# Kernel optimization log

Measured on AMD Instinct MI355X. Metric: run time of the kernel, lower is better.

The kernel has to match this reference:

```python
import jax, jax.numpy as jnp
import numpy as np

B, N, F_IN, F_OUT = 4, 4096, 64, 64
ALPHA = 0.2   # leakyrelu negative slope
M_MIX = 0.8   # self.m
NEG_INF = -1e12


def setup_inputs() -> dict:
    key = jax.random.key(0)
    k1, k2, k3, k4 = jax.random.split(key, 4)
    inp = jax.random.normal(k1, (B, N, F_IN), dtype=jnp.float32)
    adj = jax.random.uniform(k2, (B, N, N), dtype=jnp.float32)
    # xavier_uniform with gain=1.414
    limW = 1.414 * np.sqrt(6.0 / (F_IN + F_OUT))
    W = jax.random.uniform(k3, (F_IN, F_OUT), dtype=jnp.float32, minval=-limW, maxval=limW)
    lima = 1.414 * np.sqrt(6.0 / (2 * F_OUT + 1))
    a = jax.random.uniform(k4, (2 * F_OUT, 1), dtype=jnp.float32, minval=-lima, maxval=lima)
    return {"inp": inp, "adj": adj, "W": W, "a": a}


def reference(inp, adj, W, a):
    # h: [B, N, F_OUT]
    h = jnp.einsum("bnf,fo->bno", inp, W)
    # The torch code builds a_input[b,i,j] = [h_i ; h_j], applies leakyrelu
    # elementwise, then contracts with a. Since leakyrelu is elementwise,
    # e[b,i,j] = lrelu(h_i) @ a[:F] + lrelu(h_j) @ a[F:], exactly.
    lh = jax.nn.leaky_relu(h, negative_slope=ALPHA)          # [B, N, F_OUT]
    f_src = lh @ a[:F_OUT, 0]                                # [B, N]  (h_i term)
    f_dst = lh @ a[F_OUT:, 0]                                # [B, N]  (h_j term)
    e = f_src[:, :, None] + f_dst[:, None, :]                # [B, N, N]
    dj = M_MIX * adj + (1.0 - M_MIX) * e
    attention = jnp.where(dj > 0, dj, NEG_INF)
    # torch softmax over dim=1 (the i axis)
    attention = jax.nn.softmax(attention, axis=1)
    # dropout is identity in eval mode
    h_prime = jnp.einsum("bij,bjo->bio", attention, h)       # [B, N, F_OUT]
    return jax.nn.relu(h_prime)
```

## Files before the change

kernel.cpp:

```cpp
#include <hip/hip_runtime.h>
#include <hip/hip_bf16.h>


#define Bn 4
#define Nn 4096
#define JS 4

typedef _Float16 half8 __attribute__((ext_vector_type(8)));
typedef _Float16 half4 __attribute__((ext_vector_type(4)));
typedef float f32x4 __attribute__((ext_vector_type(4)));

__global__ __launch_bounds__(256) void k_prep(
    const float* __restrict__ inp, const float* __restrict__ W,
    const float* __restrict__ a, float* __restrict__ h,
    float* __restrict__ fsrc, float* __restrict__ fdst) {
  __shared__ float Ws[64 * 64];
  __shared__ float as[128];
  __shared__ float xs[4][64];
  const int t = threadIdx.x;
  for (int k = t; k < 4096; k += 256) Ws[k] = W[k];
  if (t < 128) as[t] = a[t];
  const int w = t >> 6;
  const int o = t & 63;
  const int row = blockIdx.x * 4 + w;
  xs[w][o] = inp[(size_t)row * 64 + o];
  __syncthreads();
  float acc = 0.f;
  const float* xr = xs[w];
#pragma unroll
  for (int f = 0; f < 64; ++f) acc += xr[f] * Ws[f * 64 + o];
  h[(size_t)row * 64 + o] = acc;
  float lh = acc > 0.f ? acc : 0.2f * acc;
  float vs = lh * as[o];
  float vd = lh * as[64 + o];
#pragma unroll
  for (int off = 32; off > 0; off >>= 1) {
    vs += __shfl_down(vs, off);
    vd += __shfl_down(vd, off);
  }
  if (o == 0) { fsrc[row] = vs; fdst[row] = vd; }
}

__global__ __launch_bounds__(256) void k_colstats(
    const float* __restrict__ adj, const float* __restrict__ fsrc,
    const float* __restrict__ fdst, float* __restrict__ s) {
  const int t = threadIdx.x;
  const int jb = blockIdx.x, ch = blockIdx.y, b = blockIdx.z;
  const int j = jb * 1024 + t * 4;
  __shared__ float fss[128];
  if (t < 128) fss[t] = fsrc[b * Nn + ch * 128 + t];
  __syncthreads();
  const float4 fd = *(const float4*)&fdst[b * Nn + j];
  const float4* ap = (const float4*)(adj + ((size_t)(b * Nn + ch * 128)) * Nn + j);
  float s0 = 0.f, s1 = 0.f, s2 = 0.f, s3 = 0.f;
#pragma unroll 4
  for (int ii = 0; ii < 128; ++ii) {
    float4 v = ap[(size_t)ii * 1024];
    float fi = fss[ii];
    float d0 = 0.8f * v.x + 0.2f * (fi + fd.x);
    float d1 = 0.8f * v.y + 0.2f * (fi + fd.y);
    float d2 = 0.8f * v.z + 0.2f * (fi + fd.z);
    float d3 = 0.8f * v.w + 0.2f * (fi + fd.w);
    s0 += d0 > 0.f ? __expf(d0) : 0.f;
    s1 += d1 > 0.f ? __expf(d1) : 0.f;
    s2 += d2 > 0.f ? __expf(d2) : 0.f;
    s3 += d3 > 0.f ? __expf(d3) : 0.f;
  }
  atomicAdd(&s[b * Nn + j + 0], s0);
  atomicAdd(&s[b * Nn + j + 1], s1);
  atomicAdd(&s[b * Nn + j + 2], s2);
  atomicAdd(&s[b * Nn + j + 3], s3);
}

__global__ __launch_bounds__(256) void k_hscale(
    const float* __restrict__ h, const float* __restrict__ s,
    _Float16* __restrict__ hT) {
  const int t = threadIdx.x;
  const int jt = blockIdx.x, b = blockIdx.y;
  __shared__ _Float16 hl[64][72];
#pragma unroll
  for (int r = 0; r < 4; ++r) {
    const int jl = r * 16 + (t >> 4);
    const int j = jt * 64 + jl;
    const int o4 = (t & 15) * 4;
    float sv = s[b * Nn + j];
    float si = sv > 0.f ? 1.0f / sv : 0.f;
    float4 hv = *(const float4*)&h[((size_t)(b * Nn + j)) * 64 + o4];
    hl[o4 + 0][jl] = (_Float16)(hv.x * si);
    hl[o4 + 1][jl] = (_Float16)(hv.y * si);
    hl[o4 + 2][jl] = (_Float16)(hv.z * si);
    hl[o4 + 3][jl] = (_Float16)(hv.w * si);
  }
  __syncthreads();
#pragma unroll
  for (int r = 0; r < 2; ++r) {
    const int o = r * 32 + (t >> 3);
    const int ch = t & 7;
    half8 v = *(half8*)&hl[o][ch * 8];
    *(half8*)&hT[((size_t)(b * 64 + o)) * 4096 + jt * 64 + ch * 8] = v;
  }
}

__global__ __launch_bounds__(256) void k_attnmm(
    const float* __restrict__ adj, const _Float16* __restrict__ hT,
    const float* __restrict__ fsrc, const float* __restrict__ fdst,
    float* __restrict__ part) {
  const int t = threadIdx.x;
  const int js = blockIdx.x;
  const int ib = blockIdx.y;
  const int b = blockIdx.z;
  const int i0 = ib * 128;
  const int w = t >> 6;
  const int lane = t & 63;

  __shared__ _Float16 Es[128][72];
  __shared__ _Float16 hTs[64][72];
  __shared__ float fss[128];

  if (t < 128) fss[t] = fsrc[b * Nn + i0 + t];

  f32x4 acc[2][4];
#pragma unroll
  for (int mf = 0; mf < 2; ++mf)
#pragma unroll
    for (int nt = 0; nt < 4; ++nt)
#pragma unroll
      for (int r = 0; r < 4; ++r) acc[mf][nt][r] = 0.f;

  const int jq = t & 15;
  const int ir = t >> 4;

  for (int jt = 0; jt < 16; ++jt) {
    const int j0 = js * 1024 + jt * 64;
    __syncthreads();
    const float4 fd = *(const float4*)&fdst[b * Nn + j0 + jq * 4];
    const float4* ap = (const float4*)(adj + ((size_t)(b * Nn + i0)) * Nn + j0 + jq * 4);
#pragma unroll
    for (int p = 0; p < 8; ++p) {
      const int i = p * 16 + ir;
      float4 v = ap[(size_t)i * 1024];
      float fi = fss[i];
      float d0 = 0.8f * v.x + 0.2f * (fi + fd.x);
      float d1 = 0.8f * v.y + 0.2f * (fi + fd.y);
      float d2 = 0.8f * v.z + 0.2f * (fi + fd.z);
      float d3 = 0.8f * v.w + 0.2f * (fi + fd.w);
      half4 e;
      e[0] = (_Float16)(d0 > 0.f ? __expf(d0) : 0.f);
      e[1] = (_Float16)(d1 > 0.f ? __expf(d1) : 0.f);
      e[2] = (_Float16)(d2 > 0.f ? __expf(d2) : 0.f);
      e[3] = (_Float16)(d3 > 0.f ? __expf(d3) : 0.f);
      *(half4*)&Es[i][jq * 4] = e;
    }
#pragma unroll
    for (int pp = 0; pp < 2; ++pp) {
      const int o = pp * 32 + (t >> 3);
      const int ch = t & 7;
      half8 v = *(const half8*)&hT[((size_t)(b * 64 + o)) * 4096 + j0 + ch * 8];
      *(half8*)&hTs[o][ch * 8] = v;
    }
    __syncthreads();
#pragma unroll
    for (int kh = 0; kh < 2; ++kh) {
      const int kc = (lane >> 4) * 8 + kh * 32;
      half8 a0 = *(const half8*)&Es[w * 32 + (lane & 15)][kc];
      half8 a1 = *(const half8*)&Es[w * 32 + 16 + (lane & 15)][kc];
#pragma unroll
      for (int nt = 0; nt < 4; ++nt) {
        half8 bf = *(const half8*)&hTs[nt * 16 + (lane & 15)][kc];
        acc[0][nt] = __builtin_amdgcn_mfma_f32_16x16x32_f16(a0, bf, acc[0][nt], 0, 0, 0);
        acc[1][nt] = __builtin_amdgcn_mfma_f32_16x16x32_f16(a1, bf, acc[1][nt], 0, 0, 0);
      }
    }
  }
#pragma unroll
  for (int mf = 0; mf < 2; ++mf)
#pragma unroll
    for (int nt = 0; nt < 4; ++nt)
#pragma unroll
      for (int r = 0; r < 4; ++r) {
        const int i = i0 + w * 32 + mf * 16 + (lane >> 4) * 4 + r;
        const int o = nt * 16 + (lane & 15);
        part[(((size_t)js * Bn + b) * Nn + i) * 64 + o] = acc[mf][nt][r];
      }
}

__global__ __launch_bounds__(256) void k_final(
    const float* __restrict__ part, float* __restrict__ out) {
  const int e = blockIdx.x * 256 + threadIdx.x;
  const float4* p4 = (const float4*)part;
  float4 sv = p4[e];
  const size_t stride = (size_t)Bn * Nn * 64 / 4;
#pragma unroll
  for (int js = 1; js < JS; ++js) {
    float4 v = p4[(size_t)js * stride + e];
    sv.x += v.x; sv.y += v.y; sv.z += v.z; sv.w += v.w;
  }
  float4 r;
  r.x = fmaxf(sv.x, 0.f); r.y = fmaxf(sv.y, 0.f);
  r.z = fmaxf(sv.z, 0.f); r.w = fmaxf(sv.w, 0.f);
  ((float4*)out)[e] = r;
}

extern "C" void kernel_launch(void* const* d_in, const int* in_sizes, int n_in,
                              void* d_out, int out_size, void* d_ws, size_t ws_size,
                              hipStream_t stream) {
  const float* inp = (const float*)d_in[0];
  const float* adj = (const float*)d_in[1];
  const float* W   = (const float*)d_in[2];
  const float* a   = (const float*)d_in[3];
  float* out = (float*)d_out;

  float* ws   = (float*)d_ws;
  float* h    = ws;
  float* fsrc = h + 1048576;
  float* fdst = fsrc + 16384;
  float* s    = fdst + 16384;
  float* part = s + 16384;
  _Float16* hT = (_Float16*)(part + (size_t)JS * 1048576);

  hipMemsetAsync(s, 0, 16384 * sizeof(float), stream);
  k_prep<<<Bn * Nn / 4, 256, 0, stream>>>(inp, W, a, h, fsrc, fdst);
  k_colstats<<<dim3(4, 32, Bn), 256, 0, stream>>>(adj, fsrc, fdst, s);
  k_hscale<<<dim3(64, Bn), 256, 0, stream>>>(h, s, hT);
  k_attnmm<<<dim3(JS, 32, Bn), 256, 0, stream>>>(adj, hT, fsrc, fdst, part);
  k_final<<<Bn * Nn * 64 / 4 / 256, 256, 0, stream>>>(part, out);
}
```

Before: 479.8 us.

## Materialize fp16 exp scores once in stats pass and drop split-K reduction

The column-statistics kernel now also writes the exponentiated attention scores as an fp16 matrix E. The matmul kernel then reads E directly from global memory instead of re-reading the fp32 adjacency and recomputing the exponentials. The split-K partial buffers and the final reduction kernel are removed; the matmul now covers the full K range per block and applies the ReLU itself. The aim is to avoid computing the exponentials twice and to cut the partial-sum traffic. In exchange it adds a full N×N fp16 write and read, and the matmul grid shrinks to 256 blocks whose A-operand loads come straight from global memory without LDS staging.

```diff
diff --git a/kernel.cpp b/kernel.cpp
--- a/kernel.cpp
+++ b/kernel.cpp
@@ -4,7 +4,6 @@
 
 #define Bn 4
 #define Nn 4096
-#define JS 4
 
 typedef _Float16 half8 __attribute__((ext_vector_type(8)));
 typedef _Float16 half4 __attribute__((ext_vector_type(4)));
@@ -41,30 +40,38 @@
   if (o == 0) { fsrc[row] = vs; fdst[row] = vd; }
 }
 
-__global__ __launch_bounds__(256) void k_colstats(
+__global__ __launch_bounds__(256) void k_estats(
     const float* __restrict__ adj, const float* __restrict__ fsrc,
-    const float* __restrict__ fdst, float* __restrict__ s) {
+    const float* __restrict__ fdst, _Float16* __restrict__ E,
+    float* __restrict__ s) {
   const int t = threadIdx.x;
-  const int jb = blockIdx.x, ch = blockIdx.y, b = blockIdx.z;
+  const int jb = blockIdx.x, ic = blockIdx.y, b = blockIdx.z;
   const int j = jb * 1024 + t * 4;
-  __shared__ float fss[128];
-  if (t < 128) fss[t] = fsrc[b * Nn + ch * 128 + t];
+  const int i0 = ic * 64;
+  __shared__ float fss[64];
+  if (t < 64) fss[t] = fsrc[b * Nn + i0 + t];
   __syncthreads();
   const float4 fd = *(const float4*)&fdst[b * Nn + j];
-  const float4* ap = (const float4*)(adj + ((size_t)(b * Nn + ch * 128)) * Nn + j);
+  const float4* ap = (const float4*)(adj + ((size_t)(b * Nn + i0)) * Nn + j);
+  _Float16* ep = E + ((size_t)(b * Nn + i0)) * Nn + j;
   float s0 = 0.f, s1 = 0.f, s2 = 0.f, s3 = 0.f;
 #pragma unroll 4
-  for (int ii = 0; ii < 128; ++ii) {
+  for (int ii = 0; ii < 64; ++ii) {
     float4 v = ap[(size_t)ii * 1024];
     float fi = fss[ii];
     float d0 = 0.8f * v.x + 0.2f * (fi + fd.x);
     float d1 = 0.8f * v.y + 0.2f * (fi + fd.y);
     float d2 = 0.8f * v.z + 0.2f * (fi + fd.z);
     float d3 = 0.8f * v.w + 0.2f * (fi + fd.w);
-    s0 += d0 > 0.f ? __expf(d0) : 0.f;
-    s1 += d1 > 0.f ? __expf(d1) : 0.f;
-    s2 += d2 > 0.f ? __expf(d2) : 0.f;
-    s3 += d3 > 0.f ? __expf(d3) : 0.f;
+    float e0 = d0 > 0.f ? __expf(d0) : 0.f;
+    float e1 = d1 > 0.f ? __expf(d1) : 0.f;
+    float e2 = d2 > 0.f ? __expf(d2) : 0.f;
+    float e3 = d3 > 0.f ? __expf(d3) : 0.f;
+    s0 += e0; s1 += e1; s2 += e2; s3 += e3;
+    half4 e;
+    e[0] = (_Float16)e0; e[1] = (_Float16)e1;
+    e[2] = (_Float16)e2; e[3] = (_Float16)e3;
+    *(half4*)(ep + (size_t)ii * Nn) = e;
   }
   atomicAdd(&s[b * Nn + j + 0], s0);
   atomicAdd(&s[b * Nn + j + 1], s1);
@@ -102,103 +109,57 @@
 }
 
 __global__ __launch_bounds__(256) void k_attnmm(
-    const float* __restrict__ adj, const _Float16* __restrict__ hT,
-    const float* __restrict__ fsrc, const float* __restrict__ fdst,
-    float* __restrict__ part) {
+    const _Float16* __restrict__ E, const _Float16* __restrict__ hT,
+    float* __restrict__ out) {
   const int t = threadIdx.x;
-  const int js = blockIdx.x;
-  const int ib = blockIdx.y;
-  const int b = blockIdx.z;
-  const int i0 = ib * 128;
+  const int ib = blockIdx.x;
+  const int b = blockIdx.y;
+  const int i0 = ib * 64;
   const int w = t >> 6;
   const int lane = t & 63;
 
-  __shared__ _Float16 Es[128][72];
-  __shared__ _Float16 hTs[64][72];
-  __shared__ float fss[128];
+  __shared__ _Float16 hs[64][264];
 
-  if (t < 128) fss[t] = fsrc[b * Nn + i0 + t];
+  f32x4 acc[4];
+#pragma unroll
+  for (int nt = 0; nt < 4; ++nt)
+#pragma unroll
+    for (int r = 0; r < 4; ++r) acc[nt][r] = 0.f;
 
-  f32x4 acc[2][4];
+  const int ai = i0 + w * 16 + (lane & 15);
+  const int ko = (lane >> 4) * 8;
+  const _Float16* Erow = E + ((size_t)(b * Nn + ai)) * Nn;
+  const int so = t >> 2;
+  const int sk = (t & 3) * 64;
+  const _Float16* hTrow = hT + ((size_t)(b * 64 + so)) * Nn + sk;
+
+  for (int ch = 0; ch < 16; ++ch) {
+    const int k0 = ch * 256;
+    __syncthreads();
 #pragma unroll
-  for (int mf = 0; mf < 2; ++mf)
-#pragma unroll
-    for (int nt = 0; nt < 4; ++nt)
-#pragma unroll
-      for (int r = 0; r < 4; ++r) acc[mf][nt][r] = 0.f;
-
-  const int jq = t & 15;
-  const int ir = t >> 4;
-
-  for (int jt = 0; jt < 16; ++jt) {
-    const int j0 = js * 1024 + jt * 64;
-    __syncthreads();
-    const float4 fd = *(const float4*)&fdst[b * Nn + j0 + jq * 4];
-    const float4* ap = (const float4*)(adj + ((size_t)(b * Nn + i0)) * Nn + j0 + jq * 4);
-#pragma unroll
-    for (int p = 0; p < 8; ++p) {
-      const int i = p * 16 + ir;
-      float4 v = ap[(size_t)i * 1024];
-      float fi = fss[i];
-      float d0 = 0.8f * v.x + 0.2f * (fi + fd.x);
-      float d1 = 0.8f * v.y + 0.2f * (fi + fd.y);
-      float d2 = 0.8f * v.z + 0.2f * (fi + fd.z);
-      float d3 = 0.8f * v.w + 0.2f * (fi + fd.w);
-      half4 e;
-      e[0] = (_Float16)(d0 > 0.f ? __expf(d0) : 0.f);
-      e[1] = (_Float16)(d1 > 0.f ? __expf(d1) : 0.f);
-      e[2] = (_Float16)(d2 > 0.f ? __expf(d2) : 0.f);
-      e[3] = (_Float16)(d3 > 0.f ? __expf(d3) : 0.f);
-      *(half4*)&Es[i][jq * 4] = e;
-    }
-#pragma unroll
-    for (int pp = 0; pp < 2; ++pp) {
-      const int o = pp * 32 + (t >> 3);
-      const int ch = t & 7;
-      half8 v = *(const half8*)&hT[((size_t)(b * 64 + o)) * 4096 + j0 + ch * 8];
-      *(half8*)&hTs[o][ch * 8] = v;
+    for (int q = 0; q < 8; ++q) {
+      half8 v = *(const half8*)(hTrow + k0 + q * 8);
+      *(half8*)&hs[so][sk + q * 8] = v;
     }
     __syncthreads();
 #pragma unroll
-    for (int kh = 0; kh < 2; ++kh) {
-      const int kc = (lane >> 4) * 8 + kh * 32;
-      half8 a0 = *(const half8*)&Es[w * 32 + (lane & 15)][kc];
-      half8 a1 = *(const half8*)&Es[w * 32 + 16 + (lane & 15)][kc];
+    for (int kt = 0; kt < 8; ++kt) {
+      half8 af = *(const half8*)(Erow + k0 + kt * 32 + ko);
 #pragma unroll
       for (int nt = 0; nt < 4; ++nt) {
-        half8 bf = *(const half8*)&hTs[nt * 16 + (lane & 15)][kc];
-        acc[0][nt] = __builtin_amdgcn_mfma_f32_16x16x32_f16(a0, bf, acc[0][nt], 0, 0, 0);
-        acc[1][nt] = __builtin_amdgcn_mfma_f32_16x16x32_f16(a1, bf, acc[1][nt], 0, 0, 0);
+        half8 bf = *(const half8*)&hs[nt * 16 + (lane & 15)][kt * 32 + ko];
+        acc[nt] = __builtin_amdgcn_mfma_f32_16x16x32_f16(af, bf, acc[nt], 0, 0, 0);
       }
     }
   }
 #pragma unroll
-  for (int mf = 0; mf < 2; ++mf)
+  for (int nt = 0; nt < 4; ++nt)
 #pragma unroll
-    for (int nt = 0; nt < 4; ++nt)
-#pragma unroll
-      for (int r = 0; r < 4; ++r) {
-        const int i = i0 + w * 32 + mf * 16 + (lane >> 4) * 4 + r;
-        const int o = nt * 16 + (lane & 15);
-        part[(((size_t)js * Bn + b) * Nn + i) * 64 + o] = acc[mf][nt][r];
-      }
-}
-
-__global__ __launch_bounds__(256) void k_final(
-    const float* __restrict__ part, float* __restrict__ out) {
-  const int e = blockIdx.x * 256 + threadIdx.x;
-  const float4* p4 = (const float4*)part;
-  float4 sv = p4[e];
-  const size_t stride = (size_t)Bn * Nn * 64 / 4;
-#pragma unroll
-  for (int js = 1; js < JS; ++js) {
-    float4 v = p4[(size_t)js * stride + e];
-    sv.x += v.x; sv.y += v.y; sv.z += v.z; sv.w += v.w;
-  }
-  float4 r;
-  r.x = fmaxf(sv.x, 0.f); r.y = fmaxf(sv.y, 0.f);
-  r.z = fmaxf(sv.z, 0.f); r.w = fmaxf(sv.w, 0.f);
-  ((float4*)out)[e] = r;
+    for (int r = 0; r < 4; ++r) {
+      const int i = i0 + w * 16 + (lane >> 4) * 4 + r;
+      const int o = nt * 16 + (lane & 15);
+      out[((size_t)(b * Nn + i)) * 64 + o] = fmaxf(acc[nt][r], 0.f);
+    }
 }
 
 extern "C" void kernel_launch(void* const* d_in, const int* in_sizes, int n_in,
@@ -215,13 +176,12 @@
   float* fsrc = h + 1048576;
   float* fdst = fsrc + 16384;
   float* s    = fdst + 16384;
-  float* part = s + 16384;
-  _Float16* hT = (_Float16*)(part + (size_t)JS * 1048576);
+  _Float16* hT = (_Float16*)(s + 16384);
+  _Float16* E  = hT + (size_t)1048576;
 
   hipMemsetAsync(s, 0, 16384 * sizeof(float), stream);
   k_prep<<<Bn * Nn / 4, 256, 0, stream>>>(inp, W, a, h, fsrc, fdst);
-  k_colstats<<<dim3(4, 32, Bn), 256, 0, stream>>>(adj, fsrc, fdst, s);
+  k_estats<<<dim3(4, 64, Bn), 256, 0, stream>>>(adj, fsrc, fdst, E, s);
   k_hscale<<<dim3(64, Bn), 256, 0, stream>>>(h, s, hT);
-  k_attnmm<<<dim3(JS, 32, Bn), 256, 0, stream>>>(adj, hT, fsrc, fdst, part);
-  k_final<<<Bn * Nn * 64 / 4 / 256, 256, 0, stream>>>(part, out);
+  k_attnmm<<<dim3(64, Bn), 256, 0, stream>>>(E, hT, out);
 }
```

After: 475.6 us. Within noise of the previous version (-0.9%).
